# Kernel optimization log

Measured on AMD Instinct MI355X. Metric: run time of the kernel, lower is better.

The kernel has to match this reference:

```python
import jax, jax.numpy as jnp
import numpy as np

N = 100000      # nodes
E = 1600000     # edges
F_IN = 64       # node_features
F_OUT = 32      # output_size


def _cheb2(H, row, col, w_norm, theta, bias):
    # ChebConv K=2, sym normalization, lambda_max=2 (GCLSTM default):
    # L_hat = L - I = -D^{-1/2} A D^{-1/2}, so T0 = H, T1 = -A_norm H
    agg = jax.ops.segment_sum(w_norm[:, None] * H[col], row, num_segments=N)  # [N, F_OUT]
    return H @ theta[0] - agg @ theta[1] + bias


def setup_inputs() -> dict:
    key = jax.random.key(0)
    ks = jax.random.split(key, 24)
    inp = {}
    inp["x"] = jax.random.normal(ks[0], (N, F_IN), jnp.float32)
    inp["edge_index"] = jax.random.randint(ks[1], (2, E), 0, N)
    inp["edge_weight"] = jax.random.uniform(ks[2], (E,), jnp.float32)
    inp["h"] = jax.random.normal(ks[3], (N, F_OUT), jnp.float32)
    inp["c"] = jax.random.normal(ks[4], (N, F_OUT), jnp.float32)
    s_in = float(1.0 / np.sqrt(F_IN))
    s_out = float(1.0 / np.sqrt(F_OUT))
    i = 5
    for g in "ifco":
        inp[f"W_{g}"] = jax.random.uniform(ks[i], (F_IN, F_OUT), jnp.float32, -s_in, s_in); i += 1
        inp[f"b_{g}"] = jax.random.uniform(ks[i], (1, F_OUT), jnp.float32, -s_in, s_in); i += 1
        inp[f"theta_{g}"] = jax.random.uniform(ks[i], (2, F_OUT, F_OUT), jnp.float32, -s_out, s_out); i += 1
        inp[f"cb_{g}"] = jax.random.uniform(ks[i], (F_OUT,), jnp.float32, -s_out, s_out); i += 1
    inp["W_lin"] = jax.random.uniform(ks[i], (F_OUT, 1), jnp.float32, -s_out, s_out); i += 1
    inp["b_lin"] = jax.random.uniform(ks[i], (1,), jnp.float32, -s_out, s_out)
    return inp


def reference(x, edge_index, edge_weight, h, c,
              W_i, b_i, theta_i, cb_i,
              W_f, b_f, theta_f, cb_f,
              W_c, b_c, theta_c, cb_c,
              W_o, b_o, theta_o, cb_o,
              W_lin, b_lin):
    row, col = edge_index[0], edge_index[1]
    # symmetric normalization of edge weights (get_laplacian 'sym')
    deg = jax.ops.segment_sum(edge_weight, row, num_segments=N)
    dis = jnp.where(deg > 0, jax.lax.rsqrt(jnp.where(deg > 0, deg, 1.0)), 0.0)
    w_norm = dis[row] * edge_weight * dis[col]  # [E]
    # GCLSTM gates: input x through dense W, hidden h through ChebConv
    I = jax.nn.sigmoid(x @ W_i + _cheb2(h, row, col, w_norm, theta_i, cb_i) + b_i)
    Fg = jax.nn.sigmoid(x @ W_f + _cheb2(h, row, col, w_norm, theta_f, cb_f) + b_f)
    T = jnp.tanh(x @ W_c + _cheb2(h, row, col, w_norm, theta_c, cb_c) + b_c)
    C = Fg * c + I * T
    O = jax.nn.sigmoid(x @ W_o + _cheb2(h, row, col, w_norm, theta_o, cb_o) + b_o)
    H = O * jnp.tanh(C)
    # wrapper head: relu then Linear(out, 1)
    return jax.nn.relu(H) @ W_lin + b_lin  # [N, 1]
```

## Files before the change

kernel.cpp:

```cpp
#include <hip/hip_runtime.h>
#include <math.h>

#define NN 100000
#define NE 1600000
#define BSH 6
#define BMSK 63
#define NBUK 1563
#define CAP 1280
#define NSB 391
#define EPC 4096

typedef __attribute__((ext_vector_type(8))) short bf16x8;
typedef __attribute__((ext_vector_type(4))) float f32x4;

#define MFMA(A, B, C) __builtin_amdgcn_mfma_f32_16x16x32_bf16(A, B, C, 0, 0, 0)

__device__ __forceinline__ float sigm(float z) { return 1.0f / (1.0f + expf(-z)); }

__device__ __forceinline__ void split1(float v, unsigned short* hi, unsigned short* lo) {
  unsigned u = __float_as_uint(v);
  *hi = (unsigned short)(u >> 16);
  float hf = __uint_as_float(u & 0xFFFF0000u);
  float lf = v - hf;
  *lo = (unsigned short)(__float_as_uint(lf) >> 16);
}

__device__ __forceinline__ void split8(const float* f, bf16x8* hi, bf16x8* lo) {
#pragma unroll
  for (int j = 0; j < 8; ++j) {
    unsigned short h, l;
    split1(f[j], &h, &l);
    (*hi)[j] = (short)h;
    (*lo)[j] = (short)l;
  }
}

__device__ __forceinline__ bf16x8 as_bf16x8(uint4 q) {
  union { uint4 q; bf16x8 v; } u;
  u.q = q;
  return u.v;
}

__device__ __forceinline__ void load8(const float4* p, int idx4, float* f) {
  float4 a = p[idx4];
  float4 b = p[idx4 + 1];
  f[0] = a.x; f[1] = a.y; f[2] = a.z; f[3] = a.w;
  f[4] = b.x; f[5] = b.y; f[6] = b.z; f[7] = b.w;
}


__global__ __launch_bounds__(256) void k_scat(const int* __restrict__ row,
                                              const int* __restrict__ col,
                                              const float* __restrict__ ew,
                                              int* __restrict__ cursor,
                                              int2* __restrict__ colw) {
  __shared__ int hist[NBUK];
  const int t = threadIdx.x;
  const int bid = blockIdx.x;
  for (int i = t; i < NBUK; i += 256) hist[i] = 0;
  __syncthreads();
  const int e0 = bid * EPC;
  const int e1 = min(e0 + EPC, NE);
  for (int e = e0 + t; e < e1; e += 256)
    atomicAdd(&hist[row[e] >> BSH], 1);
  __syncthreads();
  const int off = (bid * 61) % NBUK;
  for (int i0 = t; i0 < NBUK; i0 += 256) {
    int i = i0 + off;
    if (i >= NBUK) i -= NBUK;
    int h = hist[i];
    if (h > 0) hist[i] = atomicAdd(&cursor[i], h);
  }
  __syncthreads();
  for (int e = e0 + t; e < e1; e += 256) {
    int r = row[e];
    int c = col[e];
    float w = ew[e];
    int b = r >> BSH;
    int slot = atomicAdd(&hist[b], 1);
    if (slot < CAP)
      colw[b * CAP + slot] = make_int2(c | ((r & BMSK) << 17), __float_as_int(w));
  }
}

struct DegParams {
  const int* cursor;
  const int2* colw;
  float* dis;
  const float* W[4];
  const float* T0[4];
  const float* T1[4];
  const float* bsrc[4];
  const float* cb[4];
  uint4* fh;
  uint4* fl;
  float* bias;
};

__global__ __launch_bounds__(256) void k_deg(DegParams p) {
  const int t = threadIdx.x;
  const int bid = blockIdx.x;
  if (bid >= NBUK) {
    int ex = bid - NBUK;
    if (ex < 8) {
      int idx = ex * 256 + t;
      int T = idx >> 6;
      int lane = idx & 63;
      int ncol = ((T & 7) * 16) + (lane & 15);
      int g = ncol >> 5;
      int c = ncol & 31;
      int kq = (lane >> 4) * 8;
      const float* mat;
      int kbase;
      if (T < 16) { mat = p.W[g]; kbase = (T >> 3) * 32 + kq; }
      else if (T < 24) { mat = p.T0[g]; kbase = kq; }
      else { mat = p.T1[g]; kbase = kq; }
      unsigned hw[4], lw[4];
#pragma unroll
      for (int jj = 0; jj < 4; ++jj) {
        unsigned short h0, l0, h1, l1;
        split1(mat[(kbase + 2 * jj) * 32 + c], &h0, &l0);
        split1(mat[(kbase + 2 * jj + 1) * 32 + c], &h1, &l1);
        hw[jj] = (unsigned)h0 | ((unsigned)h1 << 16);
        lw[jj] = (unsigned)l0 | ((unsigned)l1 << 16);
      }
      p.fh[idx] = make_uint4(hw[0], hw[1], hw[2], hw[3]);
      p.fl[idx] = make_uint4(lw[0], lw[1], lw[2], lw[3]);
    } else if (t < 128) {
      p.bias[t] = p.bsrc[t >> 5][t & 31] + p.cb[t >> 5][t & 31];
    }
    return;
  }
  __shared__ float dg[64];
  if (t < 64) dg[t] = 0.0f;
  __syncthreads();
  const int M = min(p.cursor[bid], CAP);
  const int base = bid * CAP;
  for (int i = t; i < M; i += 256) {
    int2 e = p.colw[base + i];
    atomicAdd(&dg[e.x >> 17], __int_as_float(e.y));
  }
  __syncthreads();
  int node = (bid << BSH) + t;
  if (t < 64 && node < NN) {
    float d = dg[t];
    p.dis[node] = d > 0.0f ? rsqrtf(d) : 0.0f;
  }
}

struct FusedParams {
  const float4* x4;
  const float4* h4;
  const float* cst;
  const int* cursor;
  const int2* colw;
  const float* dis;
  const uint4* fh;
  const uint4* fl;
  const float* bias;
  const float* wlin;
  const float* blin;
  float* out;
};

__global__ __launch_bounds__(256) void k_fused(FusedParams p) {
  __shared__ int2 stage[CAP];
  __shared__ int cnt[64], excl[64], cur64[64];
  __shared__ int s[256];
  const int t = threadIdx.x;
  const int b = blockIdx.x;
  const int nbase = b << BSH;
  if (t < 64) cnt[t] = 0;
  __syncthreads();

  const int base = b * CAP;
  const int M = min(p.cursor[b], CAP);
  for (int i = t; i < M; i += 256)
    atomicAdd(&cnt[p.colw[base + i].x >> 17], 1);
  __syncthreads();
  {
    int v = (t < 64) ? cnt[t] : 0;
    s[t] = v;
    __syncthreads();
    for (int o = 1; o < 64; o <<= 1) {
      int a = (t >= o) ? s[t - o] : 0;
      __syncthreads();
      s[t] += a;
      __syncthreads();
    }
    if (t < 64) {
      excl[t] = s[t] - v;
      cur64[t] = s[t] - v;
    }
  }
  __syncthreads();
  for (int i = t; i < M; i += 256) {
    int2 e = p.colw[base + i];
    int rl = e.x >> 17;
    int c = e.x & 0x1FFFF;
    float w = __int_as_float(e.y) * p.dis[c];
    int slot = atomicAdd(&cur64[rl], 1);
    stage[slot] = make_int2(c, __float_as_int(w));
  }
  __syncthreads();

  const int lane = t & 63;
  const int wv = t >> 6;
  const int mr = lane & 15;
  const int quad = lane >> 4;
  const int m0 = nbase + wv * 16;
  int m = m0 + mr;
  if (m >= NN) m = NN - 1;
  const int rlh = m - nbase;

  bf16x8 xh[2], xl[2], hh, hl, gh, gl;
  float f[8];
#pragma unroll
  for (int kt = 0; kt < 2; ++kt) {
    load8(p.x4, (m * 64 + kt * 32 + quad * 8) >> 2, f);
    split8(f, &xh[kt], &xl[kt]);
  }
  load8(p.h4, (m * 32 + quad * 8) >> 2, f);
  split8(f, &hh, &hl);

  float fa[8] = {0.f, 0.f, 0.f, 0.f, 0.f, 0.f, 0.f, 0.f};
  float fb[8] = {0.f, 0.f, 0.f, 0.f, 0.f, 0.f, 0.f, 0.f};
  {
    int s0 = excl[rlh];
    int rem = cnt[rlh];
    int j = 0;
    for (; j + 3 < rem; j += 4) {
      int2 w0 = stage[s0 + j], w1 = stage[s0 + j + 1];
      int2 w2 = stage[s0 + j + 2], w3 = stage[s0 + j + 3];
      const float4* h0 = p.h4 + (w0.x * 8 + quad * 2);
      const float4* h1 = p.h4 + (w1.x * 8 + quad * 2);
      const float4* h2 = p.h4 + (w2.x * 8 + quad * 2);
      const float4* h3 = p.h4 + (w3.x * 8 + quad * 2);
      float4 a0 = h0[0], a1 = h0[1];
      float4 b0 = h1[0], b1 = h1[1];
      float4 c0 = h2[0], c1 = h2[1];
      float4 d0 = h3[0], d1 = h3[1];
      float f0 = __int_as_float(w0.y), f1 = __int_as_float(w1.y);
      float f2 = __int_as_float(w2.y), f3 = __int_as_float(w3.y);
      fa[0] = fmaf(f0, a0.x, fa[0]); fa[1] = fmaf(f0, a0.y, fa[1]);
      fa[2] = fmaf(f0, a0.z, fa[2]); fa[3] = fmaf(f0, a0.w, fa[3]);
      fa[4] = fmaf(f0, a1.x, fa[4]); fa[5] = fmaf(f0, a1.y, fa[5]);
      fa[6] = fmaf(f0, a1.z, fa[6]); fa[7] = fmaf(f0, a1.w, fa[7]);
      fb[0] = fmaf(f1, b0.x, fb[0]); fb[1] = fmaf(f1, b0.y, fb[1]);
      fb[2] = fmaf(f1, b0.z, fb[2]); fb[3] = fmaf(f1, b0.w, fb[3]);
      fb[4] = fmaf(f1, b1.x, fb[4]); fb[5] = fmaf(f1, b1.y, fb[5]);
      fb[6] = fmaf(f1, b1.z, fb[6]); fb[7] = fmaf(f1, b1.w, fb[7]);
      fa[0] = fmaf(f2, c0.x, fa[0]); fa[1] = fmaf(f2, c0.y, fa[1]);
      fa[2] = fmaf(f2, c0.z, fa[2]); fa[3] = fmaf(f2, c0.w, fa[3]);
      fa[4] = fmaf(f2, c1.x, fa[4]); fa[5] = fmaf(f2, c1.y, fa[5]);
      fa[6] = fmaf(f2, c1.z, fa[6]); fa[7] = fmaf(f2, c1.w, fa[7]);
      fb[0] = fmaf(f3, d0.x, fb[0]); fb[1] = fmaf(f3, d0.y, fb[1]);
      fb[2] = fmaf(f3, d0.z, fb[2]); fb[3] = fmaf(f3, d0.w, fb[3]);
      fb[4] = fmaf(f3, d1.x, fb[4]); fb[5] = fmaf(f3, d1.y, fb[5]);
      fb[6] = fmaf(f3, d1.z, fb[6]); fb[7] = fmaf(f3, d1.w, fb[7]);
    }
    for (; j < rem; ++j) {
      int2 cw = stage[s0 + j];
      const float4* hp = p.h4 + (cw.x * 8 + quad * 2);
      float4 a0 = hp[0], a1 = hp[1];
      float w = __int_as_float(cw.y);
      fa[0] = fmaf(w, a0.x, fa[0]); fa[1] = fmaf(w, a0.y, fa[1]);
      fa[2] = fmaf(w, a0.z, fa[2]); fa[3] = fmaf(w, a0.w, fa[3]);
      fa[4] = fmaf(w, a1.x, fa[4]); fa[5] = fmaf(w, a1.y, fa[5]);
      fa[6] = fmaf(w, a1.z, fa[6]); fa[7] = fmaf(w, a1.w, fa[7]);
    }
  }
  {
    float dn = -p.dis[m];
#pragma unroll
    for (int j = 0; j < 8; ++j) f[j] = dn * (fa[j] + fb[j]);
    split8(f, &gh, &gl);
  }

  float wl0 = p.wlin[mr];
  float wl1 = p.wlin[mr + 16];
  float bl = p.blin[0];

  f32x4 acc[8];
#pragma unroll 2
  for (int nt = 0; nt < 8; ++nt) {
    float bv = p.bias[nt * 16 + mr];
    f32x4 a;
    a[0] = bv; a[1] = bv; a[2] = bv; a[3] = bv;
    bf16x8 b0h = as_bf16x8(p.fh[nt * 64 + lane]);
    bf16x8 b0l = as_bf16x8(p.fl[nt * 64 + lane]);
    bf16x8 b1h = as_bf16x8(p.fh[(8 + nt) * 64 + lane]);
    bf16x8 b1l = as_bf16x8(p.fl[(8 + nt) * 64 + lane]);
    bf16x8 t0h = as_bf16x8(p.fh[(16 + nt) * 64 + lane]);
    bf16x8 t0l = as_bf16x8(p.fl[(16 + nt) * 64 + lane]);
    bf16x8 t1h = as_bf16x8(p.fh[(24 + nt) * 64 + lane]);
    bf16x8 t1l = as_bf16x8(p.fl[(24 + nt) * 64 + lane]);
    a = MFMA(xh[0], b0h, a); a = MFMA(xh[0], b0l, a); a = MFMA(xl[0], b0h, a);
    a = MFMA(xh[1], b1h, a); a = MFMA(xh[1], b1l, a); a = MFMA(xl[1], b1h, a);
    a = MFMA(hh, t0h, a);    a = MFMA(hh, t0l, a);    a = MFMA(hl, t0h, a);
    a = MFMA(gh, t1h, a);    a = MFMA(gh, t1l, a);    a = MFMA(gl, t1h, a);
    acc[nt] = a;
  }

#pragma unroll
  for (int r = 0; r < 4; ++r) {
    int node = m0 + quad * 4 + r;
    int nc = node < NN ? node : NN - 1;
    float c0 = p.cst[nc * 32 + mr];
    float c1 = p.cst[nc * 32 + 16 + mr];
    float I0 = sigm(acc[0][r]), I1 = sigm(acc[1][r]);
    float F0 = sigm(acc[2][r]), F1 = sigm(acc[3][r]);
    float T0 = tanhf(acc[4][r]), T1 = tanhf(acc[5][r]);
    float O0 = sigm(acc[6][r]), O1 = sigm(acc[7][r]);
    float C0 = fmaf(F0, c0, I0 * T0);
    float C1 = fmaf(F1, c1, I1 * T1);
    float H0 = O0 * tanhf(C0);
    float H1 = O1 * tanhf(C1);
    float part = fmaf(fmaxf(H0, 0.f), wl0, fmaxf(H1, 0.f) * wl1);
#pragma unroll
    for (int sh = 1; sh < 16; sh <<= 1) part += __shfl_xor(part, sh, 64);
    if (mr == 0 && node < NN) p.out[node] = part + bl;
  }
}

extern "C" void kernel_launch(void* const* d_in, const int* in_sizes, int n_in,
                              void* d_out, int out_size, void* d_ws, size_t ws_size,
                              hipStream_t stream) {
  const float* x = (const float*)d_in[0];
  const int* row = (const int*)d_in[1];
  const int* col = row + NE;
  const float* ew = (const float*)d_in[2];
  const float* h = (const float*)d_in[3];
  const float* c = (const float*)d_in[4];

  float* ws = (float*)d_ws;
  float* dis = ws;
  int* cursor = (int*)(ws + 100000);
  uint4* fh = (uint4*)(ws + 101568);
  uint4* fl = (uint4*)(ws + 109760);
  float* biasws = ws + 117952;
  int2* colw = (int2*)(ws + 118080);

  hipMemsetAsync(cursor, 0, NBUK * sizeof(int), stream);
  k_scat<<<NSB, 256, 0, stream>>>(row, col, ew, cursor, colw);

  DegParams dp;
  dp.cursor = cursor;
  dp.colw = colw;
  dp.dis = dis;
  for (int g = 0; g < 4; ++g) {
    dp.W[g] = (const float*)d_in[5 + 4 * g];
    dp.bsrc[g] = (const float*)d_in[6 + 4 * g];
    dp.T0[g] = (const float*)d_in[7 + 4 * g];
    dp.T1[g] = dp.T0[g] + 1024;
    dp.cb[g] = (const float*)d_in[8 + 4 * g];
  }
  dp.fh = fh;
  dp.fl = fl;
  dp.bias = biasws;
  k_deg<<<NBUK + 9, 256, 0, stream>>>(dp);

  FusedParams fp;
  fp.x4 = (const float4*)x;
  fp.h4 = (const float4*)h;
  fp.cst = c;
  fp.cursor = cursor;
  fp.colw = colw;
  fp.dis = dis;
  fp.fh = fh;
  fp.fl = fl;
  fp.bias = biasws;
  fp.wlin = (const float*)d_in[21];
  fp.blin = (const float*)d_in[22];
  fp.out = (float*)d_out;
  k_fused<<<NBUK, 256, 0, stream>>>(fp);
}
```

Before: 260.8 us.

## Use 128-node buckets with half-bucket fused blocks and fast-math activations

Result: no change. 260.6 us (-0.1%).

```diff
diff --git a/kernel.cpp b/kernel.cpp
--- a/kernel.cpp
+++ b/kernel.cpp
@@ -3,19 +3,21 @@
 
 #define NN 100000
 #define NE 1600000
-#define BSH 6
-#define BMSK 63
-#define NBUK 1563
-#define CAP 1280
+#define BSH 7
+#define BMSK 127
+#define NBUK 782
+#define CAP 2560
 #define NSB 391
 #define EPC 4096
+#define CAPH 1536
 
 typedef __attribute__((ext_vector_type(8))) short bf16x8;
 typedef __attribute__((ext_vector_type(4))) float f32x4;
 
 #define MFMA(A, B, C) __builtin_amdgcn_mfma_f32_16x16x32_bf16(A, B, C, 0, 0, 0)
 
-__device__ __forceinline__ float sigm(float z) { return 1.0f / (1.0f + expf(-z)); }
+__device__ __forceinline__ float fsigm(float z) { return 1.0f / (1.0f + __expf(-z)); }
+__device__ __forceinline__ float ftanh(float z) { return 1.0f - 2.0f / (__expf(2.0f * z) + 1.0f); }
 
 __device__ __forceinline__ void split1(float v, unsigned short* hi, unsigned short* lo) {
   unsigned u = __float_as_uint(v);
@@ -131,8 +133,8 @@
     }
     return;
   }
-  __shared__ float dg[64];
-  if (t < 64) dg[t] = 0.0f;
+  __shared__ float dg[128];
+  if (t < 128) dg[t] = 0.0f;
   __syncthreads();
   const int M = min(p.cursor[bid], CAP);
   const int base = bid * CAP;
@@ -142,7 +144,7 @@
   }
   __syncthreads();
   int node = (bid << BSH) + t;
-  if (t < 64 && node < NN) {
+  if (t < 128 && node < NN) {
     float d = dg[t];
     p.dis[node] = d > 0.0f ? rsqrtf(d) : 0.0f;
   }
@@ -164,19 +166,24 @@
 };
 
 __global__ __launch_bounds__(256) void k_fused(FusedParams p) {
-  __shared__ int2 stage[CAP];
+  __shared__ int2 stage[CAPH];
   __shared__ int cnt[64], excl[64], cur64[64];
   __shared__ int s[256];
   const int t = threadIdx.x;
-  const int b = blockIdx.x;
-  const int nbase = b << BSH;
+  const int jb = blockIdx.x;
+  const int b = jb >> 1;
+  const int hf = jb & 1;
+  const int nbase = (b << BSH) + (hf << 6);
+  if (nbase >= NN) return;
   if (t < 64) cnt[t] = 0;
   __syncthreads();
 
   const int base = b * CAP;
   const int M = min(p.cursor[b], CAP);
-  for (int i = t; i < M; i += 256)
-    atomicAdd(&cnt[p.colw[base + i].x >> 17], 1);
+  for (int i = t; i < M; i += 256) {
+    int rl = p.colw[base + i].x >> 17;
+    if ((rl >> 6) == hf) atomicAdd(&cnt[rl & 63], 1);
+  }
   __syncthreads();
   {
     int v = (t < 64) ? cnt[t] : 0;
@@ -197,10 +204,12 @@
   for (int i = t; i < M; i += 256) {
     int2 e = p.colw[base + i];
     int rl = e.x >> 17;
-    int c = e.x & 0x1FFFF;
-    float w = __int_as_float(e.y) * p.dis[c];
-    int slot = atomicAdd(&cur64[rl], 1);
-    stage[slot] = make_int2(c, __float_as_int(w));
+    if ((rl >> 6) == hf) {
+      int c = e.x & 0x1FFFF;
+      float w = __int_as_float(e.y) * p.dis[c];
+      int slot = atomicAdd(&cur64[rl & 63], 1);
+      if (slot < CAPH) stage[slot] = make_int2(c, __float_as_int(w));
+    }
   }
   __syncthreads();
 
@@ -308,14 +317,14 @@
     int nc = node < NN ? node : NN - 1;
     float c0 = p.cst[nc * 32 + mr];
     float c1 = p.cst[nc * 32 + 16 + mr];
-    float I0 = sigm(acc[0][r]), I1 = sigm(acc[1][r]);
-    float F0 = sigm(acc[2][r]), F1 = sigm(acc[3][r]);
-    float T0 = tanhf(acc[4][r]), T1 = tanhf(acc[5][r]);
-    float O0 = sigm(acc[6][r]), O1 = sigm(acc[7][r]);
+    float I0 = fsigm(acc[0][r]), I1 = fsigm(acc[1][r]);
+    float F0 = fsigm(acc[2][r]), F1 = fsigm(acc[3][r]);
+    float T0 = ftanh(acc[4][r]), T1 = ftanh(acc[5][r]);
+    float O0 = fsigm(acc[6][r]), O1 = fsigm(acc[7][r]);
     float C0 = fmaf(F0, c0, I0 * T0);
     float C1 = fmaf(F1, c1, I1 * T1);
-    float H0 = O0 * tanhf(C0);
-    float H1 = O1 * tanhf(C1);
+    float H0 = O0 * ftanh(C0);
+    float H1 = O1 * ftanh(C1);
     float part = fmaf(fmaxf(H0, 0.f), wl0, fmaxf(H1, 0.f) * wl1);
 #pragma unroll
     for (int sh = 1; sh < 16; sh <<= 1) part += __shfl_xor(part, sh, 64);
@@ -336,10 +345,10 @@
   float* ws = (float*)d_ws;
   float* dis = ws;
   int* cursor = (int*)(ws + 100000);
-  uint4* fh = (uint4*)(ws + 101568);
-  uint4* fl = (uint4*)(ws + 109760);
-  float* biasws = ws + 117952;
-  int2* colw = (int2*)(ws + 118080);
+  uint4* fh = (uint4*)(ws + 100800);
+  uint4* fl = (uint4*)(ws + 108992);
+  float* biasws = ws + 117184;
+  int2* colw = (int2*)(ws + 117312);
 
   hipMemsetAsync(cursor, 0, NBUK * sizeof(int), stream);
   k_scat<<<NSB, 256, 0, stream>>>(row, col, ew, cursor, colw);
@@ -373,5 +382,5 @@
   fp.wlin = (const float*)d_in[21];
   fp.blin = (const float*)d_in[22];
   fp.out = (float*)d_out;
-  k_fused<<<NBUK, 256, 0, stream>>>(fp);
-}
+  k_fused<<<2 * NBUK, 256, 0, stream>>>(fp);
+}
```
